# Kernel optimization log

Hardware: AMD Instinct MI355X
Metric: run time of the kernel (lower is better)

The kernel has to match this reference:

```python
import jax, jax.numpy as jnp
import numpy as np

N = 50000      # nodes
E = 800000     # edges
D_IN, D_HID, D_MID, D_OUT = 128, 128, 30, 64  # layer dims (30 hard-coded in module)
NEG_SLOPE = 0.01  # F.leaky_relu default

def _w(key, shape, scale=0.05):
    return jax.random.normal(key, shape, dtype=jnp.float32) * scale

def setup_inputs() -> dict:
    key = jax.random.key(0)
    ks = jax.random.split(key, 24)
    inp = {
        "x": jax.random.normal(ks[0], (N, D_IN), jnp.float32),
        "e": jax.random.normal(ks[1], (E, D_IN), jnp.float32),
        "src": jax.random.randint(ks[2], (E,), 0, N, jnp.int32),
        "dst": jax.random.randint(ks[3], (E,), 0, N, jnp.int32),
    }
    dims = [(D_IN, D_HID), (D_HID, D_MID), (D_MID, D_OUT)]
    i = 4
    for l, (di, do) in enumerate(dims, 1):
        inp[f"W_n{l}"] = _w(ks[i], (di, do)); i += 1
        inp[f"b_n{l}"] = jnp.zeros((do,), jnp.float32)
        inp[f"W_ni{l}"] = _w(ks[i], (di, do)); i += 1
        inp[f"W_nj{l}"] = _w(ks[i], (di, do)); i += 1
        inp[f"W_f{l}"] = _w(ks[i], (di, do)); i += 1
        inp[f"attn{l}"] = _w(ks[i], (do,)); i += 1
        inp[f"bias{l}"] = jnp.zeros((do,), jnp.float32)
    return inp

def _egat_layer(x, e, src, dst, W_n, b_n, W_ni, W_nj, W_f, attn, bias):
    n = x.shape[0]
    # edge features: f_ij = leaky_relu(fc_ni(x)_i + fc_nj(x)_j + fc_fij(e) + bias)
    f = (x @ W_ni)[src] + (x @ W_nj)[dst] + e @ W_f + bias
    f = jax.nn.leaky_relu(f, negative_slope=NEG_SLOPE)          # [E, do]
    score = jnp.sum(f * attn, axis=-1)                           # [E]
    # edge_softmax: softmax of scores over edges sharing a destination node
    m = jax.ops.segment_max(score, dst, num_segments=n)
    ex = jnp.exp(score - m[dst])
    s = jax.ops.segment_sum(ex, dst, num_segments=n)
    a = ex / s[dst]                                              # [E]
    # attention-weighted aggregation of transformed source nodes
    h = x @ W_n + b_n                                            # [N, do]
    h_out = jax.ops.segment_sum(h[src] * a[:, None], dst, num_segments=n)
    return h_out, f

def reference(x, e, src, dst,
              W_n1, b_n1, W_ni1, W_nj1, W_f1, attn1, bias1,
              W_n2, b_n2, W_ni2, W_nj2, W_f2, attn2, bias2,
              W_n3, b_n3, W_ni3, W_nj3, W_f3, attn3, bias3):
    h, f = _egat_layer(x, e, src, dst, W_n1, b_n1, W_ni1, W_nj1, W_f1, attn1, bias1)
    h, f = _egat_layer(h, f, src, dst, W_n2, b_n2, W_ni2, W_nj2, W_f2, attn2, bias2)
    h, f = _egat_layer(h, f, src, dst, W_n3, b_n3, W_ni3, W_nj3, W_f3, attn3, bias3)
    # num_heads == 1, so out_edge_feats[:, 0, :] == f  -> [E, D_OUT]
    return f
```

## Files before the change

kernel.cpp:

```cpp
#include <hip/hip_runtime.h>
#include <math.h>

#define NTH 256

__device__ __forceinline__ unsigned enc_f(float x){
  unsigned u = __float_as_uint(x);
  return (u & 0x80000000u) ? ~u : (u | 0x80000000u);
}
__device__ __forceinline__ float dec_f(unsigned v){
  unsigned u = (v & 0x80000000u) ? (v & 0x7FFFFFFFu) : ~v;
  return __uint_as_float(u);
}

template<int DI, int DIS, int DO, int DOS, int JSPLIT, int MINW>
__global__ __launch_bounds__(NTH, MINW) void node_linear_k(
    const float* __restrict__ x, const float* __restrict__ W,
    const float* __restrict__ bias, float* __restrict__ out, int N)
{
  constexpr int WPB = NTH / 64;
  constexpr int GPB = WPB / JSPLIT;
  constexpr int DOW = DO / JSPLIT;
  const int lane = threadIdx.x & 63;
  const int wave = threadIdx.x >> 6;
  const int group = blockIdx.x * GPB + (wave / JSPLIT);
  const int j0 = __builtin_amdgcn_readfirstlane((wave % JSPLIT) * DOW);
  const int row = group * 64 + lane;
  const bool valid = row < N;
  const int rr = valid ? row : (N - 1);
  const float* xr = x + (size_t)rr * DIS;

  float acc[DOW];
  if (bias != nullptr) {
    #pragma unroll
    for (int j = 0; j < DOW; j++) acc[j] = bias[j0 + j];
  } else {
    #pragma unroll
    for (int j = 0; j < DOW; j++) acc[j] = 0.f;
  }

  constexpr int K4 = DI & ~3;
  for (int k = 0; k < K4; k += 4) {
    float4 ev = *(const float4*)(xr + k);
    float ea[4] = {ev.x, ev.y, ev.z, ev.w};
    #pragma unroll
    for (int kk = 0; kk < 4; kk++) {
      const float* wr = W + (size_t)(k + kk) * DO + j0;
      #pragma unroll
      for (int j = 0; j < DOW; j++)
        acc[j] = fmaf(ea[kk], wr[j], acc[j]);
    }
  }
  #pragma unroll
  for (int k = K4; k < DI; k++) {
    float ev = xr[k];
    const float* wr = W + (size_t)k * DO + j0;
    #pragma unroll
    for (int j = 0; j < DOW; j++)
      acc[j] = fmaf(ev, wr[j], acc[j]);
  }

  if (valid) {
    float* orow = out + (size_t)row * DOS + j0;
    constexpr int J4 = DOW & ~3;
    #pragma unroll
    for (int j = 0; j < J4; j += 4)
      *(float4*)(orow + j) = make_float4(acc[j], acc[j+1], acc[j+2], acc[j+3]);
    #pragma unroll
    for (int j = J4; j < DOW; j++) orow[j] = acc[j];
  }
}

template<int DI, int DIS, int DO, int DOS, int JSPLIT, bool SCORE, int MINW>
__global__ __launch_bounds__(NTH, MINW) void edge_f_k(
    const float* __restrict__ efeat, const float* __restrict__ xWni,
    const float* __restrict__ xWnj, const float* __restrict__ Wf,
    const float* __restrict__ attn, const float* __restrict__ bias,
    const int* __restrict__ src, const int* __restrict__ dst,
    float* __restrict__ fout, float* __restrict__ score,
    unsigned* __restrict__ menc, int E)
{
  constexpr int WPB = NTH / 64;
  constexpr int GPB = WPB / JSPLIT;
  constexpr int DOW = DO / JSPLIT;
  const int lane = threadIdx.x & 63;
  const int wave = threadIdx.x >> 6;
  const int sub  = wave % JSPLIT;
  const int group = blockIdx.x * GPB + (wave / JSPLIT);
  const int j0 = __builtin_amdgcn_readfirstlane(sub * DOW);
  const int eidx = group * 64 + lane;
  const bool valid = eidx < E;
  const int ee = valid ? eidx : (E - 1);

  const int sn = src[ee];
  const int dn = dst[ee];
  const float* ar = xWni + (size_t)sn * DOS + j0;
  const float* br = xWnj + (size_t)dn * DOS + j0;

  float acc[DOW];
  constexpr int J4 = DOW & ~3;
  #pragma unroll
  for (int j = 0; j < J4; j += 4) {
    float4 a4 = *(const float4*)(ar + j);
    float4 b4 = *(const float4*)(br + j);
    acc[j+0] = bias[j0+j+0] + a4.x + b4.x;
    acc[j+1] = bias[j0+j+1] + a4.y + b4.y;
    acc[j+2] = bias[j0+j+2] + a4.z + b4.z;
    acc[j+3] = bias[j0+j+3] + a4.w + b4.w;
  }
  #pragma unroll
  for (int j = J4; j < DOW; j++)
    acc[j] = bias[j0+j] + ar[j] + br[j];

  const float* er = efeat + (size_t)ee * DIS;
  constexpr int K4 = DI & ~3;
  for (int k = 0; k < K4; k += 4) {
    float4 ev = *(const float4*)(er + k);
    float ea[4] = {ev.x, ev.y, ev.z, ev.w};
    #pragma unroll
    for (int kk = 0; kk < 4; kk++) {
      const float* wr = Wf + (size_t)(k + kk) * DO + j0;
      #pragma unroll
      for (int j = 0; j < DOW; j++)
        acc[j] = fmaf(ea[kk], wr[j], acc[j]);
    }
  }
  #pragma unroll
  for (int k = K4; k < DI; k++) {
    float ev = er[k];
    const float* wr = Wf + (size_t)k * DO + j0;
    #pragma unroll
    for (int j = 0; j < DOW; j++)
      acc[j] = fmaf(ev, wr[j], acc[j]);
  }

  float sc = 0.f;
  #pragma unroll
  for (int j = 0; j < DOW; j++) {
    float v = acc[j];
    v = (v > 0.f) ? v : 0.01f * v;
    acc[j] = v;
    if (SCORE) sc += v * attn[j0 + j];
  }

  if (valid) {
    float* orow = fout + (size_t)eidx * DOS + j0;
    #pragma unroll
    for (int j = 0; j < J4; j += 4)
      *(float4*)(orow + j) = make_float4(acc[j], acc[j+1], acc[j+2], acc[j+3]);
    #pragma unroll
    for (int j = J4; j < DOW; j++) orow[j] = acc[j];
  }

  if constexpr (SCORE && JSPLIT > 1) {
    __shared__ float scpart[WPB][64];
    scpart[wave][lane] = sc;
    __syncthreads();
    if (sub == 0 && valid) {
      float tot = sc;
      #pragma unroll
      for (int s = 1; s < JSPLIT; s++) tot += scpart[wave + s][lane];
      score[eidx] = tot;
      atomicMax(&menc[dn], enc_f(tot));
    }
  } else if constexpr (SCORE) {
    if (valid) {
      score[eidx] = sc;
      atomicMax(&menc[dn], enc_f(sc));
    }
  }
}

__global__ __launch_bounds__(NTH) void softmax_ex_k(float* __restrict__ score,
    const int* __restrict__ dst, const unsigned* __restrict__ menc,
    float* __restrict__ ssum, int E)
{
  int i = blockIdx.x * NTH + threadIdx.x;
  if (i < E) {
    int d = dst[i];
    float ex = expf(score[i] - dec_f(menc[d]));
    score[i] = ex;
    atomicAdd(&ssum[d], ex);
  }
}

__global__ __launch_bounds__(NTH) void softmax_norm_k(float* __restrict__ score,
    const float* __restrict__ ssum, const int* __restrict__ dst, int E)
{
  int i = blockIdx.x * NTH + threadIdx.x;
  if (i < E) score[i] = score[i] / ssum[dst[i]];
}

template<int DO, int HS, int OS>
__global__ __launch_bounds__(NTH) void scatter_h_k(const float* __restrict__ a,
    const int* __restrict__ src, const int* __restrict__ dst,
    const float* __restrict__ h, float* __restrict__ hout, int E)
{
  long long idx = (long long)blockIdx.x * NTH + threadIdx.x;
  if (idx < (long long)E * DO) {
    int e = (int)(idx / DO);
    int col = (int)(idx - (long long)e * DO);
    atomicAdd(&hout[(size_t)dst[e] * OS + col], h[(size_t)src[e] * HS + col] * a[e]);
  }
}

extern "C" void kernel_launch(void* const* d_in, const int* in_sizes, int n_in,
                              void* d_out, int out_size, void* d_ws, size_t ws_size,
                              hipStream_t stream)
{
  const float* x    = (const float*)d_in[0];
  const float* e    = (const float*)d_in[1];
  const int*   src  = (const int*)d_in[2];
  const int*   dst  = (const int*)d_in[3];
  const float* W_n1 = (const float*)d_in[4];   const float* b_n1  = (const float*)d_in[5];
  const float* W_ni1= (const float*)d_in[6];   const float* W_nj1 = (const float*)d_in[7];
  const float* W_f1 = (const float*)d_in[8];   const float* attn1 = (const float*)d_in[9];
  const float* bias1= (const float*)d_in[10];
  const float* W_n2 = (const float*)d_in[11];  const float* b_n2  = (const float*)d_in[12];
  const float* W_ni2= (const float*)d_in[13];  const float* W_nj2 = (const float*)d_in[14];
  const float* W_f2 = (const float*)d_in[15];  const float* attn2 = (const float*)d_in[16];
  const float* bias2= (const float*)d_in[17];
  const float* W_n3 = (const float*)d_in[18];  const float* b_n3  = (const float*)d_in[19];
  const float* W_ni3= (const float*)d_in[20];  const float* W_nj3 = (const float*)d_in[21];
  const float* W_f3 = (const float*)d_in[22];  const float* attn3 = (const float*)d_in[23];
  const float* bias3= (const float*)d_in[24];
  (void)W_n3; (void)b_n3;

  const int N = in_sizes[0] / 128;
  const int E = in_sizes[2];

  float* ws = (float*)d_ws;
  size_t off = 0;
  float* fbuf1 = ws + off; off += (size_t)E * 128;
  float* fbuf2 = ws + off; off += (size_t)E * 32;
  float* xWni  = ws + off; off += (size_t)N * 128;
  float* xWnj  = ws + off; off += (size_t)N * 128;
  float* hbuf  = ws + off; off += (size_t)N * 128;
  float* nodeA = ws + off; off += (size_t)N * 128;
  float* nodeB = ws + off; off += (size_t)N * 32;
  float* scoreb= ws + off; off += (size_t)E;
  unsigned* menc = (unsigned*)(ws + off); off += (size_t)N;
  float* sbuf  = ws + off; off += (size_t)N;

  const int groupsN = (N + 63) / 64;
  const int groupsE = (E + 63) / 64;
  const int gN2 = (groupsN + 1) / 2;
  const int gN4 = (groupsN + 3) / 4;
  const int gE2 = (groupsE + 1) / 2;
  const int gE4 = (groupsE + 3) / 4;
  const int gEe = (E + NTH - 1) / NTH;

  node_linear_k<128,128,128,128,2,4><<<gN2,NTH,0,stream>>>(x, W_ni1, nullptr, xWni, N);
  node_linear_k<128,128,128,128,2,4><<<gN2,NTH,0,stream>>>(x, W_nj1, nullptr, xWnj, N);
  node_linear_k<128,128,128,128,2,4><<<gN2,NTH,0,stream>>>(x, W_n1,  b_n1,   hbuf, N);
  hipMemsetAsync(menc, 0, (size_t)N * 4, stream);
  hipMemsetAsync(sbuf, 0, (size_t)N * 4, stream);
  hipMemsetAsync(nodeA, 0, (size_t)N * 128 * 4, stream);
  edge_f_k<128,128,128,128,2,true,4><<<gE2,NTH,0,stream>>>(e, xWni, xWnj, W_f1, attn1, bias1,
                                                           src, dst, fbuf1, scoreb, menc, E);
  softmax_ex_k<<<gEe,NTH,0,stream>>>(scoreb, dst, menc, sbuf, E);
  softmax_norm_k<<<gEe,NTH,0,stream>>>(scoreb, sbuf, dst, E);
  scatter_h_k<128,128,128><<<(int)(((long long)E*128 + NTH-1)/NTH),NTH,0,stream>>>(scoreb, src, dst, hbuf, nodeA, E);

  node_linear_k<128,128,30,32,1,5><<<gN4,NTH,0,stream>>>(nodeA, W_ni2, nullptr, xWni, N);
  node_linear_k<128,128,30,32,1,5><<<gN4,NTH,0,stream>>>(nodeA, W_nj2, nullptr, xWnj, N);
  node_linear_k<128,128,30,32,1,5><<<gN4,NTH,0,stream>>>(nodeA, W_n2,  b_n2,   hbuf, N);
  hipMemsetAsync(menc, 0, (size_t)N * 4, stream);
  hipMemsetAsync(sbuf, 0, (size_t)N * 4, stream);
  hipMemsetAsync(nodeB, 0, (size_t)N * 32 * 4, stream);
  edge_f_k<128,128,30,32,1,true,5><<<gE4,NTH,0,stream>>>(fbuf1, xWni, xWnj, W_f2, attn2, bias2,
                                                         src, dst, fbuf2, scoreb, menc, E);
  softmax_ex_k<<<gEe,NTH,0,stream>>>(scoreb, dst, menc, sbuf, E);
  softmax_norm_k<<<gEe,NTH,0,stream>>>(scoreb, sbuf, dst, E);
  scatter_h_k<30,32,32><<<(int)(((long long)E*30 + NTH-1)/NTH),NTH,0,stream>>>(scoreb, src, dst, hbuf, nodeB, E);

  node_linear_k<30,32,64,64,2,4><<<gN2,NTH,0,stream>>>(nodeB, W_ni3, nullptr, xWni, N);
  node_linear_k<30,32,64,64,2,4><<<gN2,NTH,0,stream>>>(nodeB, W_nj3, nullptr, xWnj, N);
  edge_f_k<30,32,64,64,2,false,4><<<gE2,NTH,0,stream>>>(fbuf2, xWni, xWnj, W_f3, attn3, bias3,
                                                        src, dst, (float*)d_out, nullptr, nullptr, E);
}
```

Before: 2.634 ms.

## Stage edge features through LDS with 4-way output split; vectorize layer-1 scatter

```diff
diff --git a/kernel.cpp b/kernel.cpp
--- a/kernel.cpp
+++ b/kernel.cpp
@@ -70,7 +70,122 @@
   }
 }
 
-template<int DI, int DIS, int DO, int DOS, int JSPLIT, bool SCORE, int MINW>
+template<int DI, int DIS, int DOW, int DO, int DOS, bool SCORE, int MINW>
+__global__ __launch_bounds__(NTH, MINW) void edge_f_s_k(
+    const float* __restrict__ efeat, const float* __restrict__ xWni,
+    const float* __restrict__ xWnj, const float* __restrict__ Wf,
+    const float* __restrict__ attn, const float* __restrict__ bias,
+    const int* __restrict__ src, const int* __restrict__ dst,
+    float* __restrict__ fout, float* __restrict__ score,
+    unsigned* __restrict__ menc, int E)
+{
+  constexpr int KC = 32;
+  constexpr int NCH = (DI + KC - 1) / KC;
+  constexpr bool KFULL = (DI % KC == 0);
+  static_assert(KFULL || NCH == 1, "partial K chunk only supported as single chunk");
+  static_assert(4 * DOW == DO, "4 sub-waves must tile DO exactly");
+  constexpr int FPT = (64 * KC / 4) / NTH;
+
+  const int tid  = threadIdx.x;
+  const int lane = tid & 63;
+  const int sub  = tid >> 6;
+  const int j0 = __builtin_amdgcn_readfirstlane(sub * DOW);
+  const int group = blockIdx.x;
+  const int eidx = group * 64 + lane;
+  const bool valid = eidx < E;
+  const int ee = valid ? eidx : (E - 1);
+
+  __shared__ float4 et[64 * 8];
+  __shared__ float scpart[4][64];
+
+  const int sn = src[ee];
+  const int dn = dst[ee];
+  const float* ar = xWni + (size_t)sn * DOS + j0;
+  const float* br = xWnj + (size_t)dn * DOS + j0;
+
+  float acc[DOW];
+  #pragma unroll
+  for (int j = 0; j < DOW; j += 4) {
+    float4 a4 = *(const float4*)(ar + j);
+    float4 b4 = *(const float4*)(br + j);
+    acc[j+0] = bias[j0+j+0] + a4.x + b4.x;
+    acc[j+1] = bias[j0+j+1] + a4.y + b4.y;
+    acc[j+2] = bias[j0+j+2] + a4.z + b4.z;
+    acc[j+3] = bias[j0+j+3] + a4.w + b4.w;
+  }
+
+  float4 pv[FPT];
+  #pragma unroll
+  for (int i = 0; i < FPT; i++) {
+    int s = i * NTH + tid;
+    int row = s >> 3, c4 = s & 7;
+    int er = group * 64 + row; er = (er < E) ? er : (E - 1);
+    pv[i] = *(const float4*)(efeat + (size_t)er * DIS + c4 * 4);
+  }
+
+  for (int ch = 0; ch < NCH; ++ch) {
+    __syncthreads();
+    #pragma unroll
+    for (int i = 0; i < FPT; i++) {
+      int s = i * NTH + tid;
+      int row = s >> 3, c4 = s & 7;
+      et[row * 8 + (c4 ^ (row & 7))] = pv[i];
+    }
+    if (ch + 1 < NCH) {
+      #pragma unroll
+      for (int i = 0; i < FPT; i++) {
+        int s = i * NTH + tid;
+        int row = s >> 3, c4 = s & 7;
+        int er = group * 64 + row; er = (er < E) ? er : (E - 1);
+        pv[i] = *(const float4*)(efeat + (size_t)er * DIS + (ch + 1) * KC + c4 * 4);
+      }
+    }
+    __syncthreads();
+
+    #pragma unroll
+    for (int c4 = 0; c4 < 8; ++c4) {
+      if constexpr (!KFULL) { if (c4 * 4 >= DI) break; }
+      float4 ev = et[lane * 8 + (c4 ^ (lane & 7))];
+      float ea[4] = {ev.x, ev.y, ev.z, ev.w};
+      #pragma unroll
+      for (int kk = 0; kk < 4; kk++) {
+        if constexpr (!KFULL) { if (c4 * 4 + kk >= DI) break; }
+        const float* wr = Wf + (size_t)(ch * KC + c4 * 4 + kk) * DO + j0;
+        #pragma unroll
+        for (int j = 0; j < DOW; j++)
+          acc[j] = fmaf(ea[kk], wr[j], acc[j]);
+      }
+    }
+  }
+
+  float sc = 0.f;
+  #pragma unroll
+  for (int j = 0; j < DOW; j++) {
+    float v = acc[j];
+    v = (v > 0.f) ? v : 0.01f * v;
+    acc[j] = v;
+    if (SCORE) sc += v * attn[j0 + j];
+  }
+
+  if (valid) {
+    float* orow = fout + (size_t)eidx * DOS + j0;
+    #pragma unroll
+    for (int j = 0; j < DOW; j += 4)
+      *(float4*)(orow + j) = make_float4(acc[j], acc[j+1], acc[j+2], acc[j+3]);
+  }
+
+  if constexpr (SCORE) {
+    scpart[sub][lane] = sc;
+    __syncthreads();
+    if (sub == 0 && valid) {
+      float tot = scpart[0][lane] + scpart[1][lane] + scpart[2][lane] + scpart[3][lane];
+      score[eidx] = tot;
+      atomicMax(&menc[dn], enc_f(tot));
+    }
+  }
+}
+
+template<int DI, int DIS, int DO, int DOS, bool SCORE, int MINW>
 __global__ __launch_bounds__(NTH, MINW) void edge_f_k(
     const float* __restrict__ efeat, const float* __restrict__ xWni,
     const float* __restrict__ xWnj, const float* __restrict__ Wf,
@@ -79,37 +194,31 @@
     float* __restrict__ fout, float* __restrict__ score,
     unsigned* __restrict__ menc, int E)
 {
-  constexpr int WPB = NTH / 64;
-  constexpr int GPB = WPB / JSPLIT;
-  constexpr int DOW = DO / JSPLIT;
   const int lane = threadIdx.x & 63;
   const int wave = threadIdx.x >> 6;
-  const int sub  = wave % JSPLIT;
-  const int group = blockIdx.x * GPB + (wave / JSPLIT);
-  const int j0 = __builtin_amdgcn_readfirstlane(sub * DOW);
-  const int eidx = group * 64 + lane;
+  const int eidx = (blockIdx.x * (NTH >> 6) + wave) * 64 + lane;
   const bool valid = eidx < E;
   const int ee = valid ? eidx : (E - 1);
 
   const int sn = src[ee];
   const int dn = dst[ee];
-  const float* ar = xWni + (size_t)sn * DOS + j0;
-  const float* br = xWnj + (size_t)dn * DOS + j0;
-
-  float acc[DOW];
-  constexpr int J4 = DOW & ~3;
+  const float* ar = xWni + (size_t)sn * DOS;
+  const float* br = xWnj + (size_t)dn * DOS;
+
+  float acc[DO];
+  constexpr int J4 = DO & ~3;
   #pragma unroll
   for (int j = 0; j < J4; j += 4) {
     float4 a4 = *(const float4*)(ar + j);
     float4 b4 = *(const float4*)(br + j);
-    acc[j+0] = bias[j0+j+0] + a4.x + b4.x;
-    acc[j+1] = bias[j0+j+1] + a4.y + b4.y;
-    acc[j+2] = bias[j0+j+2] + a4.z + b4.z;
-    acc[j+3] = bias[j0+j+3] + a4.w + b4.w;
-  }
-  #pragma unroll
-  for (int j = J4; j < DOW; j++)
-    acc[j] = bias[j0+j] + ar[j] + br[j];
+    acc[j+0] = bias[j+0] + a4.x + b4.x;
+    acc[j+1] = bias[j+1] + a4.y + b4.y;
+    acc[j+2] = bias[j+2] + a4.z + b4.z;
+    acc[j+3] = bias[j+3] + a4.w + b4.w;
+  }
+  #pragma unroll
+  for (int j = J4; j < DO; j++)
+    acc[j] = bias[j] + ar[j] + br[j];
 
   const float* er = efeat + (size_t)ee * DIS;
   constexpr int K4 = DI & ~3;
@@ -118,52 +227,38 @@
     float ea[4] = {ev.x, ev.y, ev.z, ev.w};
     #pragma unroll
     for (int kk = 0; kk < 4; kk++) {
-      const float* wr = Wf + (size_t)(k + kk) * DO + j0;
+      const float* wr = Wf + (size_t)(k + kk) * DO;
       #pragma unroll
-      for (int j = 0; j < DOW; j++)
+      for (int j = 0; j < DO; j++)
         acc[j] = fmaf(ea[kk], wr[j], acc[j]);
     }
   }
   #pragma unroll
   for (int k = K4; k < DI; k++) {
     float ev = er[k];
-    const float* wr = Wf + (size_t)k * DO + j0;
-    #pragma unroll
-    for (int j = 0; j < DOW; j++)
+    const float* wr = Wf + (size_t)k * DO;
+    #pragma unroll
+    for (int j = 0; j < DO; j++)
       acc[j] = fmaf(ev, wr[j], acc[j]);
   }
 
   float sc = 0.f;
   #pragma unroll
-  for (int j = 0; j < DOW; j++) {
+  for (int j = 0; j < DO; j++) {
     float v = acc[j];
     v = (v > 0.f) ? v : 0.01f * v;
     acc[j] = v;
-    if (SCORE) sc += v * attn[j0 + j];
+    if (SCORE) sc += v * attn[j];
   }
 
   if (valid) {
-    float* orow = fout + (size_t)eidx * DOS + j0;
+    float* orow = fout + (size_t)eidx * DOS;
     #pragma unroll
     for (int j = 0; j < J4; j += 4)
       *(float4*)(orow + j) = make_float4(acc[j], acc[j+1], acc[j+2], acc[j+3]);
     #pragma unroll
-    for (int j = J4; j < DOW; j++) orow[j] = acc[j];
-  }
-
-  if constexpr (SCORE && JSPLIT > 1) {
-    __shared__ float scpart[WPB][64];
-    scpart[wave][lane] = sc;
-    __syncthreads();
-    if (sub == 0 && valid) {
-      float tot = sc;
-      #pragma unroll
-      for (int s = 1; s < JSPLIT; s++) tot += scpart[wave + s][lane];
-      score[eidx] = tot;
-      atomicMax(&menc[dn], enc_f(tot));
-    }
-  } else if constexpr (SCORE) {
-    if (valid) {
+    for (int j = J4; j < DO; j++) orow[j] = acc[j];
+    if constexpr (SCORE) {
       score[eidx] = sc;
       atomicMax(&menc[dn], enc_f(sc));
     }
@@ -200,6 +295,25 @@
     int e = (int)(idx / DO);
     int col = (int)(idx - (long long)e * DO);
     atomicAdd(&hout[(size_t)dst[e] * OS + col], h[(size_t)src[e] * HS + col] * a[e]);
+  }
+}
+
+template<int DO4, int HS, int OS>
+__global__ __launch_bounds__(NTH) void scatter_h4_k(const float* __restrict__ a,
+    const int* __restrict__ src, const int* __restrict__ dst,
+    const float* __restrict__ h, float* __restrict__ hout, int E)
+{
+  long long idx = (long long)blockIdx.x * NTH + threadIdx.x;
+  if (idx < (long long)E * DO4) {
+    int e = (int)(idx / DO4);
+    int c = (int)(idx - (long long)e * DO4);
+    float av = a[e];
+    float4 hv = *(const float4*)(h + (size_t)src[e] * HS + c * 4);
+    float* op = hout + (size_t)dst[e] * OS + c * 4;
+    atomicAdd(op + 0, hv.x * av);
+    atomicAdd(op + 1, hv.y * av);
+    atomicAdd(op + 2, hv.z * av);
+    atomicAdd(op + 3, hv.w * av);
   }
 }
 
@@ -245,7 +359,6 @@
   const int groupsE = (E + 63) / 64;
   const int gN2 = (groupsN + 1) / 2;
   const int gN4 = (groupsN + 3) / 4;
-  const int gE2 = (groupsE + 1) / 2;
   const int gE4 = (groupsE + 3) / 4;
   const int gEe = (E + NTH - 1) / NTH;
 
@@ -255,11 +368,11 @@
   hipMemsetAsync(menc, 0, (size_t)N * 4, stream);
   hipMemsetAsync(sbuf, 0, (size_t)N * 4, stream);
   hipMemsetAsync(nodeA, 0, (size_t)N * 128 * 4, stream);
-  edge_f_k<128,128,128,128,2,true,4><<<gE2,NTH,0,stream>>>(e, xWni, xWnj, W_f1, attn1, bias1,
-                                                           src, dst, fbuf1, scoreb, menc, E);
+  edge_f_s_k<128,128,32,128,128,true,6><<<groupsE,NTH,0,stream>>>(e, xWni, xWnj, W_f1, attn1, bias1,
+                                                                  src, dst, fbuf1, scoreb, menc, E);
   softmax_ex_k<<<gEe,NTH,0,stream>>>(scoreb, dst, menc, sbuf, E);
   softmax_norm_k<<<gEe,NTH,0,stream>>>(scoreb, sbuf, dst, E);
-  scatter_h_k<128,128,128><<<(int)(((long long)E*128 + NTH-1)/NTH),NTH,0,stream>>>(scoreb, src, dst, hbuf, nodeA, E);
+  scatter_h4_k<32,128,128><<<(int)(((long long)E*32 + NTH-1)/NTH),NTH,0,stream>>>(scoreb, src, dst, hbuf, nodeA, E);
 
   node_linear_k<128,128,30,32,1,5><<<gN4,NTH,0,stream>>>(nodeA, W_ni2, nullptr, xWni, N);
   node_linear_k<128,128,30,32,1,5><<<gN4,NTH,0,stream>>>(nodeA, W_nj2, nullptr, xWnj, N);
@@ -267,14 +380,14 @@
   hipMemsetAsync(menc, 0, (size_t)N * 4, stream);
   hipMemsetAsync(sbuf, 0, (size_t)N * 4, stream);
   hipMemsetAsync(nodeB, 0, (size_t)N * 32 * 4, stream);
-  edge_f_k<128,128,30,32,1,true,5><<<gE4,NTH,0,stream>>>(fbuf1, xWni, xWnj, W_f2, attn2, bias2,
-                                                         src, dst, fbuf2, scoreb, menc, E);
+  edge_f_k<128,128,30,32,true,5><<<gE4,NTH,0,stream>>>(fbuf1, xWni, xWnj, W_f2, attn2, bias2,
+                                                       src, dst, fbuf2, scoreb, menc, E);
   softmax_ex_k<<<gEe,NTH,0,stream>>>(scoreb, dst, menc, sbuf, E);
   softmax_norm_k<<<gEe,NTH,0,stream>>>(scoreb, sbuf, dst, E);
   scatter_h_k<30,32,32><<<(int)(((long long)E*30 + NTH-1)/NTH),NTH,0,stream>>>(scoreb, src, dst, hbuf, nodeB, E);
 
   node_linear_k<30,32,64,64,2,4><<<gN2,NTH,0,stream>>>(nodeB, W_ni3, nullptr, xWni, N);
   node_linear_k<30,32,64,64,2,4><<<gN2,NTH,0,stream>>>(nodeB, W_nj3, nullptr, xWnj, N);
-  edge_f_k<30,32,64,64,2,false,4><<<gE2,NTH,0,stream>>>(fbuf2, xWni, xWnj, W_f3, attn3, bias3,
-                                                        src, dst, (float*)d_out, nullptr, nullptr, E);
-}
+  edge_f_s_k<30,32,16,64,64,false,7><<<groupsE,NTH,0,stream>>>(fbuf2, xWni, xWnj, W_f3, attn3, bias3,
+                                                               src, dst, (float*)d_out, nullptr, nullptr, E);
+}
```

Result: slower. 3.906 ms (+48.3%).
